# Kernel optimization log

Hardware: AMD Instinct MI355X
Metric: run time of the kernel (lower is better)

Reference implementation:

```python
import jax, jax.numpy as jnp
import numpy as np

EMB_DIM = 768
HEADS = 12
HEAD_DIM = EMB_DIM // HEADS  # 64


def setup_inputs() -> dict:
    key = jax.random.key(0)
    ks = jax.random.split(key, 9)
    s = 1.0 / np.sqrt(EMB_DIM)
    d = dict(
        x=jax.random.normal(ks[0], (2, 2048, EMB_DIM), dtype=jnp.float32),
        wq_w=jax.random.normal(ks[1], (EMB_DIM, EMB_DIM), dtype=jnp.float32) * s,
        wq_b=jax.random.normal(ks[2], (EMB_DIM,), dtype=jnp.float32) * 0.01,
        wk_w=jax.random.normal(ks[3], (EMB_DIM, EMB_DIM), dtype=jnp.float32) * s,
        wk_b=jax.random.normal(ks[4], (EMB_DIM,), dtype=jnp.float32) * 0.01,
        wv_w=jax.random.normal(ks[5], (EMB_DIM, EMB_DIM), dtype=jnp.float32) * s,
        wv_b=jax.random.normal(ks[6], (EMB_DIM,), dtype=jnp.float32) * 0.01,
        wo_w=jax.random.normal(ks[7], (EMB_DIM, EMB_DIM), dtype=jnp.float32) * s,
        wo_b=jax.random.normal(ks[8], (EMB_DIM,), dtype=jnp.float32) * 0.01,
    )
    return d


def reference(x, wq_w, wq_b, wk_w, wk_b, wv_w, wv_b, wo_w, wo_b):
    b, n, _ = x.shape
    # Linear projections (torch Linear: x @ W^T + b). q scaled by 1/8 == 1/sqrt(head_dim).
    q = (x @ wq_w.T + wq_b) / 8.0
    k = x @ wk_w.T + wk_b
    v = x @ wv_w.T + wv_b
    # [b, h, n, d]
    q = q.reshape(b, n, HEADS, HEAD_DIM).transpose(0, 2, 1, 3)
    k = k.reshape(b, n, HEADS, HEAD_DIM).transpose(0, 2, 1, 3)
    v = v.reshape(b, n, HEADS, HEAD_DIM).transpose(0, 2, 1, 3)
    # Full [b, h, n, n] score matrix with causal mask (strict upper triangle = -inf)
    scores = jnp.einsum('bhqd,bhkd->bhqk', q, k)
    causal = jnp.tril(jnp.ones((n, n), dtype=bool))  # True where allowed
    scores = jnp.where(causal[None, None], scores, -jnp.inf)
    attn = jax.nn.softmax(scores, axis=-1)
    out = jnp.einsum('bhqk,bhkd->bhqd', attn, v)
    out = out.transpose(0, 2, 1, 3).reshape(b, n, EMB_DIM)
    return out @ wo_w.T + wo_b
```

## Files before the change

### kernel.cpp

```cpp
#include <hip/hip_runtime.h>
#include <hip/hip_bf16.h>
#include <math.h>

#define EMB  768
#define NH   12
#define HD   64
#define SEQ  2048
#define BATCH 2
#define NTOK 4096

typedef __attribute__((ext_vector_type(8))) short short8;
typedef __attribute__((ext_vector_type(4))) float float4v;

static __device__ __forceinline__ short f2bf(float f) {
    __hip_bfloat16 h = __float2bfloat16(f);
    return *reinterpret_cast<short*>(&h);
}

static __device__ __forceinline__ void gll16(const void* g, void* l) {
    __builtin_amdgcn_global_load_lds(
        (const __attribute__((address_space(1))) void*)g,
        (__attribute__((address_space(3))) void*)l, 16, 0, 0);
}

__global__ __launch_bounds__(256) void cast_kernel(
    const float* __restrict__ x,  const float* __restrict__ wq,
    const float* __restrict__ wk, const float* __restrict__ wv,
    const float* __restrict__ wo,
    __hip_bfloat16* __restrict__ xb,  __hip_bfloat16* __restrict__ wqb,
    __hip_bfloat16* __restrict__ wkb, __hip_bfloat16* __restrict__ wvb,
    __hip_bfloat16* __restrict__ wob)
{
    const size_t S0 = (size_t)NTOK * EMB;
    const size_t S1 = (size_t)EMB * EMB;
    size_t i = ((size_t)blockIdx.x * 256 + threadIdx.x) * 8;
    const float* src; __hip_bfloat16* dst; size_t off;
    if      (i < S0)            { src = x;  dst = xb;  off = i; }
    else if (i < S0 + S1)       { src = wq; dst = wqb; off = i - S0; }
    else if (i < S0 + 2 * S1)   { src = wk; dst = wkb; off = i - S0 - S1; }
    else if (i < S0 + 3 * S1)   { src = wv; dst = wvb; off = i - S0 - 2 * S1; }
    else                        { src = wo; dst = wob; off = i - S0 - 3 * S1; }
    float4 f0 = *(const float4*)&src[off];
    float4 f1 = *(const float4*)&src[off + 4];
    short8 o;
    o[0] = f2bf(f0.x); o[1] = f2bf(f0.y); o[2] = f2bf(f0.z); o[3] = f2bf(f0.w);
    o[4] = f2bf(f1.x); o[5] = f2bf(f1.y); o[6] = f2bf(f1.z); o[7] = f2bf(f1.w);
    *(short8*)&dst[off] = o;
}

__global__ __launch_bounds__(256) void qkv_mfma_kernel(
    const __hip_bfloat16* __restrict__ xb,
    const __hip_bfloat16* __restrict__ wqb, const float* __restrict__ bq,
    const __hip_bfloat16* __restrict__ wkb, const float* __restrict__ bk,
    const __hip_bfloat16* __restrict__ wvb, const float* __restrict__ bv,
    __hip_bfloat16* __restrict__ q, __hip_bfloat16* __restrict__ k,
    __hip_bfloat16* __restrict__ vT)
{
    __shared__ __align__(16) short As[128 * 64];
    __shared__ __align__(16) short Bs[128 * 64];
    const int t = threadIdx.x;
    const int w = t >> 6, lane = t & 63;
    const int col = lane & 15, quad = lane >> 4;
    const int wm = w >> 1, wn = w & 1;
    const int m0 = blockIdx.y * 128;
    const int mat = blockIdx.x / 6;
    const int jj0 = (blockIdx.x % 6) * 128;
    const short* X = (const short*)xb;
    const short* W = (const short*)((mat == 0) ? wqb : (mat == 1) ? wkb : wvb);
    const float* bias = (mat == 0) ? bq : (mat == 1) ? bk : bv;

    float4v acc[4][4];
    #pragma unroll
    for (int mi = 0; mi < 4; ++mi)
        #pragma unroll
        for (int ni = 0; ni < 4; ++ni) acc[mi][ni] = (float4v){0.f, 0.f, 0.f, 0.f};

    for (int kb = 0; kb < EMB; kb += 64) {
        #pragma unroll
        for (int c = 0; c < 4; ++c) {
            int I = w * 256 + c * 64 + lane;
            int row = I >> 3;
            int c8 = (I & 7) ^ (row & 7);
            gll16(X + (size_t)(m0 + row) * EMB + kb + c8 * 8,
                  &As[(w * 256 + c * 64) * 8]);
            gll16(W + (size_t)(jj0 + row) * EMB + kb + c8 * 8,
                  &Bs[(w * 256 + c * 64) * 8]);
        }
        __syncthreads();
        #pragma unroll
        for (int ks = 0; ks < 2; ++ks) {
            short8 a[4], b[4];
            #pragma unroll
            for (int mi = 0; mi < 4; ++mi) {
                int row = wm * 64 + mi * 16 + col;
                a[mi] = *(short8*)&As[row * 64 + (((ks * 4 + quad) ^ (row & 7)) * 8)];
            }
            #pragma unroll
            for (int ni = 0; ni < 4; ++ni) {
                int row = wn * 64 + ni * 16 + col;
                b[ni] = *(short8*)&Bs[row * 64 + (((ks * 4 + quad) ^ (row & 7)) * 8)];
            }
            #pragma unroll
            for (int mi = 0; mi < 4; ++mi)
                #pragma unroll
                for (int ni = 0; ni < 4; ++ni)
                    acc[mi][ni] = __builtin_amdgcn_mfma_f32_16x16x32_bf16(
                        a[mi], b[ni], acc[mi][ni], 0, 0, 0);
        }
        __syncthreads();
    }
    const float scale = (mat == 0) ? 0.125f : 1.0f;
    __hip_bfloat16* dstqk = (mat == 0) ? q : k;
    #pragma unroll
    for (int mi = 0; mi < 4; ++mi) {
        #pragma unroll
        for (int ni = 0; ni < 4; ++ni) {
            int gj = jj0 + wn * 64 + ni * 16 + col;
            int h = gj >> 6, d = gj & 63;
            float bsv = bias[gj];
            #pragma unroll
            for (int r = 0; r < 4; ++r) {
                int gm = m0 + wm * 64 + mi * 16 + quad * 4 + r;
                int bi = gm >> 11, n = gm & (SEQ - 1);
                float val = (acc[mi][ni][r] + bsv) * scale;
                if (mat == 2)
                    vT[(((size_t)bi * NH + h) * HD + d) * SEQ + n] = __float2bfloat16(val);
                else
                    dstqk[(((size_t)bi * NH + h) * SEQ + n) * HD + d] = __float2bfloat16(val);
            }
        }
    }
}

__global__ __launch_bounds__(128) void attn_mfma_kernel(
    const __hip_bfloat16* __restrict__ qg, const __hip_bfloat16* __restrict__ kg,
    const __hip_bfloat16* __restrict__ vTg, __hip_bfloat16* __restrict__ ao)
{
    __shared__ __align__(16) short Ks[2][64 * 64];
    __shared__ __align__(16) short Vt[2][64 * 64];
    __shared__ __align__(16) short Ps[2][32][72];
    const int t = threadIdx.x;
    const int w = t >> 6, lane = t & 63;
    const int col = lane & 15, quad = lane >> 4;
    const int idx = blockIdx.x;
    const int qt = 31 - idx / 24;
    const int bh = idx % 24;
    const int q0 = qt * 64;
    const size_t base = (size_t)bh * SEQ * HD;
    const short* kp = (const short*)kg + base;
    const short* vp = (const short*)vTg + base;
    const short* qp = (const short*)qg + base;

    short8 qa[2][2];
    #pragma unroll
    for (int mi = 0; mi < 2; ++mi) {
        int qrow = q0 + w * 32 + mi * 16 + col;
        #pragma unroll
        for (int ks = 0; ks < 2; ++ks)
            qa[mi][ks] = *(const short8*)&qp[(size_t)qrow * HD + ks * 32 + quad * 8];
    }
    float4v accO[2][4];
    float lacc[2][4];
    #pragma unroll
    for (int mi = 0; mi < 2; ++mi) {
        #pragma unroll
        for (int di = 0; di < 4; ++di) accO[mi][di] = (float4v){0.f, 0.f, 0.f, 0.f};
        #pragma unroll
        for (int r = 0; r < 4; ++r) lacc[mi][r] = 0.f;
    }

    #pragma unroll
    for (int c = 0; c < 4; ++c) {
        int I = w * 256 + c * 64 + lane;
        int row = I >> 3;
        int c8 = (I & 7) ^ (row & 7);
        gll16(kp + (size_t)row * HD + c8 * 8, &Ks[0][(w * 256 + c * 64) * 8]);
        gll16(vp + (size_t)row * SEQ + c8 * 8, &Vt[0][(w * 256 + c * 64) * 8]);
    }

    for (int kt = 0; kt <= qt; ++kt) {
        const int cur = kt & 1;
        const int k0 = kt * 64;
        __syncthreads();
        if (kt < qt) {
            const int kn = k0 + 64;
            #pragma unroll
            for (int c = 0; c < 4; ++c) {
                int I = w * 256 + c * 64 + lane;
                int row = I >> 3;
                int c8 = (I & 7) ^ (row & 7);
                gll16(kp + (size_t)(kn + row) * HD + c8 * 8,
                      &Ks[cur ^ 1][(w * 256 + c * 64) * 8]);
                gll16(vp + (size_t)row * SEQ + kn + c8 * 8,
                      &Vt[cur ^ 1][(w * 256 + c * 64) * 8]);
            }
        }
        const short* Kc = &Ks[cur][0];
        const short* Vc = &Vt[cur][0];

        float4v s[2][4];
        #pragma unroll
        for (int mi = 0; mi < 2; ++mi)
            #pragma unroll
            for (int ni = 0; ni < 4; ++ni) s[mi][ni] = (float4v){0.f, 0.f, 0.f, 0.f};
        #pragma unroll
        for (int ks = 0; ks < 2; ++ks)
            #pragma unroll
            for (int ni = 0; ni < 4; ++ni) {
                int row = ni * 16 + col;
                short8 kf = *(short8*)&Kc[row * 64 + (((ks * 4 + quad) ^ (row & 7)) * 8)];
                #pragma unroll
                for (int mi = 0; mi < 2; ++mi)
                    s[mi][ni] = __builtin_amdgcn_mfma_f32_16x16x32_bf16(
                        qa[mi][ks], kf, s[mi][ni], 0, 0, 0);
            }

        if (kt == qt) {
            #pragma unroll
            for (int mi = 0; mi < 2; ++mi)
                #pragma unroll
                for (int ni = 0; ni < 4; ++ni) {
                    int gcol = k0 + ni * 16 + col;
                    #pragma unroll
                    for (int r = 0; r < 4; ++r) {
                        int grow = q0 + w * 32 + mi * 16 + quad * 4 + r;
                        s[mi][ni][r] = (gcol > grow) ? 0.f : __expf(s[mi][ni][r]);
                    }
                }
        } else {
            #pragma unroll
            for (int mi = 0; mi < 2; ++mi)
                #pragma unroll
                for (int ni = 0; ni < 4; ++ni)
                    #pragma unroll
                    for (int r = 0; r < 4; ++r)
                        s[mi][ni][r] = __expf(s[mi][ni][r]);
        }
        #pragma unroll
        for (int mi = 0; mi < 2; ++mi)
            #pragma unroll
            for (int r = 0; r < 4; ++r)
                lacc[mi][r] += (s[mi][0][r] + s[mi][1][r]) + (s[mi][2][r] + s[mi][3][r]);

        #pragma unroll
        for (int mi = 0; mi < 2; ++mi)
            #pragma unroll
            for (int ni = 0; ni < 4; ++ni)
                #pragma unroll
                for (int r = 0; r < 4; ++r)
                    Ps[w][mi * 16 + quad * 4 + r][ni * 16 + col] = f2bf(s[mi][ni][r]);
        short8 pa[2][2];
        #pragma unroll
        for (int mi = 0; mi < 2; ++mi)
            #pragma unroll
            for (int ks = 0; ks < 2; ++ks)
                pa[mi][ks] = *(short8*)&Ps[w][mi * 16 + col][ks * 32 + quad * 8];

        #pragma unroll
        for (int ks = 0; ks < 2; ++ks)
            #pragma unroll
            for (int di = 0; di < 4; ++di) {
                int row = di * 16 + col;
                short8 vf = *(short8*)&Vc[row * 64 + (((ks * 4 + quad) ^ (row & 7)) * 8)];
                #pragma unroll
                for (int mi = 0; mi < 2; ++mi)
                    accO[mi][di] = __builtin_amdgcn_mfma_f32_16x16x32_bf16(
                        pa[mi][ks], vf, accO[mi][di], 0, 0, 0);
            }
    }

    #pragma unroll
    for (int msk = 1; msk < 16; msk <<= 1)
        #pragma unroll
        for (int mi = 0; mi < 2; ++mi)
            #pragma unroll
            for (int r = 0; r < 4; ++r)
                lacc[mi][r] += __shfl_xor(lacc[mi][r], msk);
    const int bi = bh / NH, h = bh % NH;
    #pragma unroll
    for (int mi = 0; mi < 2; ++mi)
        #pragma unroll
        for (int r = 0; r < 4; ++r) {
            float inv = 1.0f / lacc[mi][r];
            int n = q0 + w * 32 + mi * 16 + quad * 4 + r;
            #pragma unroll
            for (int di = 0; di < 4; ++di)
                ao[((size_t)bi * SEQ + n) * EMB + h * HD + di * 16 + col] =
                    __float2bfloat16(accO[mi][di][r] * inv);
        }
}

__global__ __launch_bounds__(256) void out_proj_mfma_kernel(
    const __hip_bfloat16* __restrict__ a, const __hip_bfloat16* __restrict__ wob,
    const float* __restrict__ bias, float* __restrict__ out)
{
    __shared__ __align__(16) short As[64 * 64];
    __shared__ __align__(16) short Bs[128 * 64];
    const int t = threadIdx.x;
    const int w = t >> 6, lane = t & 63;
    const int col = lane & 15, quad = lane >> 4;
    const int m0 = blockIdx.y * 64;
    const int n0 = blockIdx.x * 128;
    const short* A = (const short*)a;
    const short* W = (const short*)wob;

    float4v acc[4][2];
    #pragma unroll
    for (int mi = 0; mi < 4; ++mi)
        #pragma unroll
        for (int ni = 0; ni < 2; ++ni) acc[mi][ni] = (float4v){0.f, 0.f, 0.f, 0.f};

    for (int kb = 0; kb < EMB; kb += 64) {
        #pragma unroll
        for (int c = 0; c < 2; ++c) {
            int I = w * 128 + c * 64 + lane;
            int row = I >> 3;
            int c8 = (I & 7) ^ (row & 7);
            gll16(A + (size_t)(m0 + row) * EMB + kb + c8 * 8,
                  &As[(w * 128 + c * 64) * 8]);
        }
        #pragma unroll
        for (int c = 0; c < 4; ++c) {
            int I = w * 256 + c * 64 + lane;
            int row = I >> 3;
            int c8 = (I & 7) ^ (row & 7);
            gll16(W + (size_t)(n0 + row) * EMB + kb + c8 * 8,
                  &Bs[(w * 256 + c * 64) * 8]);
        }
        __syncthreads();
        #pragma unroll
        for (int ks = 0; ks < 2; ++ks) {
            short8 av[4], bv[2];
            #pragma unroll
            for (int mi = 0; mi < 4; ++mi) {
                int row = mi * 16 + col;
                av[mi] = *(short8*)&As[row * 64 + (((ks * 4 + quad) ^ (row & 7)) * 8)];
            }
            #pragma unroll
            for (int ni = 0; ni < 2; ++ni) {
                int row = w * 32 + ni * 16 + col;
                bv[ni] = *(short8*)&Bs[row * 64 + (((ks * 4 + quad) ^ (row & 7)) * 8)];
            }
            #pragma unroll
            for (int mi = 0; mi < 4; ++mi)
                #pragma unroll
                for (int ni = 0; ni < 2; ++ni)
                    acc[mi][ni] = __builtin_amdgcn_mfma_f32_16x16x32_bf16(
                        av[mi], bv[ni], acc[mi][ni], 0, 0, 0);
        }
        __syncthreads();
    }
    #pragma unroll
    for (int mi = 0; mi < 4; ++mi)
        #pragma unroll
        for (int ni = 0; ni < 2; ++ni) {
            int gj = n0 + w * 32 + ni * 16 + col;
            float bsv = bias[gj];
            #pragma unroll
            for (int r = 0; r < 4; ++r) {
                int gm = m0 + mi * 16 + quad * 4 + r;
                out[(size_t)gm * EMB + gj] = acc[mi][ni][r] + bsv;
            }
        }
}

extern "C" void kernel_launch(void* const* d_in, const int* in_sizes, int n_in,
                              void* d_out, int out_size, void* d_ws, size_t ws_size,
                              hipStream_t stream) {
    const float* x  = (const float*)d_in[0];
    const float* wq = (const float*)d_in[1];
    const float* bq = (const float*)d_in[2];
    const float* wk = (const float*)d_in[3];
    const float* bk = (const float*)d_in[4];
    const float* wv = (const float*)d_in[5];
    const float* bv = (const float*)d_in[6];
    const float* wo = (const float*)d_in[7];
    const float* bo = (const float*)d_in[8];
    float* out = (float*)d_out;

    const size_t TOK = (size_t)NTOK * EMB;
    const size_t WSZ = (size_t)EMB * EMB;
    __hip_bfloat16* xb  = (__hip_bfloat16*)d_ws;
    __hip_bfloat16* wqb = xb  + TOK;
    __hip_bfloat16* wkb = wqb + WSZ;
    __hip_bfloat16* wvb = wkb + WSZ;
    __hip_bfloat16* wob = wvb + WSZ;
    __hip_bfloat16* qb  = wob + WSZ;
    __hip_bfloat16* kb  = qb  + TOK;
    __hip_bfloat16* vTb = kb  + TOK;
    __hip_bfloat16* aob = vTb + TOK;

    cast_kernel<<<2688, 256, 0, stream>>>(x, wq, wk, wv, wo, xb, wqb, wkb, wvb, wob);
    qkv_mfma_kernel<<<dim3(18, 32), 256, 0, stream>>>(xb, wqb, bq, wkb, bk, wvb, bv,
                                                      qb, kb, vTb);
    attn_mfma_kernel<<<768, 128, 0, stream>>>(qb, kb, vTb, aob);
    out_proj_mfma_kernel<<<dim3(6, 64), 256, 0, stream>>>(aob, wob, bo, out);
}
```

Baseline: 186.2 us.

## Split long causal query tiles across two KV halves and stage V-transpose stores

Query tiles 16-31 now have their KV range split into two halves handled by separate blocks, capping per-block work at 16 KV tiles. The partial unnormalized outputs and row sums go to fp32 scratch, and a new combine kernel merges and normalizes them. This is meant to fix the load imbalance of the causal workload. Separately, the V projection epilogue transposes through LDS so the vT stores become coalesced 16-byte writes instead of scattered 2-byte ones. The cost is extra fp32 scratch traffic, one more kernel launch, and scratch buffers that reuse workspace regions.

```diff
diff --git a/kernel.cpp b/kernel.cpp
--- a/kernel.cpp
+++ b/kernel.cpp
@@ -56,8 +56,9 @@
     __hip_bfloat16* __restrict__ q, __hip_bfloat16* __restrict__ k,
     __hip_bfloat16* __restrict__ vT)
 {
-    __shared__ __align__(16) short As[128 * 64];
-    __shared__ __align__(16) short Bs[128 * 64];
+    __shared__ __align__(16) short SM[16384];
+    short* As = SM;
+    short* Bs = SM + 8192;
     const int t = threadIdx.x;
     const int w = t >> 6, lane = t & 63;
     const int col = lane & 15, quad = lane >> 4;
@@ -109,32 +110,59 @@
         }
         __syncthreads();
     }
-    const float scale = (mat == 0) ? 0.125f : 1.0f;
-    __hip_bfloat16* dstqk = (mat == 0) ? q : k;
-    #pragma unroll
-    for (int mi = 0; mi < 4; ++mi) {
-        #pragma unroll
-        for (int ni = 0; ni < 4; ++ni) {
-            int gj = jj0 + wn * 64 + ni * 16 + col;
-            int h = gj >> 6, d = gj & 63;
-            float bsv = bias[gj];
-            #pragma unroll
-            for (int r = 0; r < 4; ++r) {
-                int gm = m0 + wm * 64 + mi * 16 + quad * 4 + r;
-                int bi = gm >> 11, n = gm & (SEQ - 1);
-                float val = (acc[mi][ni][r] + bsv) * scale;
-                if (mat == 2)
-                    vT[(((size_t)bi * NH + h) * HD + d) * SEQ + n] = __float2bfloat16(val);
-                else
-                    dstqk[(((size_t)bi * NH + h) * SEQ + n) * HD + d] = __float2bfloat16(val);
-            }
+    const int bi = m0 >> 11, n0g = m0 & (SEQ - 1);
+    if (mat != 2) {
+        const float scale = (mat == 0) ? 0.125f : 1.0f;
+        __hip_bfloat16* dstqk = (mat == 0) ? q : k;
+        #pragma unroll
+        for (int mi = 0; mi < 4; ++mi) {
+            #pragma unroll
+            for (int ni = 0; ni < 4; ++ni) {
+                int gj = jj0 + wn * 64 + ni * 16 + col;
+                int h = gj >> 6, d = gj & 63;
+                float bsv = bias[gj];
+                #pragma unroll
+                for (int r = 0; r < 4; ++r) {
+                    int gm = m0 + wm * 64 + mi * 16 + quad * 4 + r;
+                    int bb = gm >> 11, n = gm & (SEQ - 1);
+                    dstqk[(((size_t)bb * NH + h) * SEQ + n) * HD + d] =
+                        __float2bfloat16((acc[mi][ni][r] + bsv) * scale);
+                }
+            }
+        }
+    } else {
+        #pragma unroll
+        for (int mi = 0; mi < 4; ++mi)
+            #pragma unroll
+            for (int ni = 0; ni < 4; ++ni) {
+                int d_l = wn * 64 + ni * 16 + col;
+                float bsv = bias[jj0 + d_l];
+                #pragma unroll
+                for (int r = 0; r < 4; ++r) {
+                    int n_l = wm * 64 + mi * 16 + quad * 4 + r;
+                    SM[(d_l << 7) + ((((n_l >> 3) ^ col) << 3) | (n_l & 7))] =
+                        f2bf(acc[mi][ni][r] + bsv);
+                }
+            }
+        __syncthreads();
+        #pragma unroll
+        for (int it = 0; it < 8; ++it) {
+            int I = it * 256 + t;
+            int d_l = I >> 4, c8 = I & 15;
+            short8 val = *(short8*)&SM[(d_l << 7) + (c8 << 3)];
+            int n_l = (c8 ^ (d_l & 15)) << 3;
+            int gj = jj0 + d_l;
+            int h = gj >> 6, dd = gj & 63;
+            *(short8*)&vT[(((size_t)bi * NH + h) * HD + dd) * SEQ + n0g + n_l] = val;
         }
     }
 }
 
 __global__ __launch_bounds__(128) void attn_mfma_kernel(
     const __hip_bfloat16* __restrict__ qg, const __hip_bfloat16* __restrict__ kg,
-    const __hip_bfloat16* __restrict__ vTg, __hip_bfloat16* __restrict__ ao)
+    const __hip_bfloat16* __restrict__ vTg, __hip_bfloat16* __restrict__ ao,
+    float* __restrict__ Os0, float* __restrict__ Os1,
+    float* __restrict__ l0, float* __restrict__ l1)
 {
     __shared__ __align__(16) short Ks[2][64 * 64];
     __shared__ __align__(16) short Vt[2][64 * 64];
@@ -142,9 +170,20 @@
     const int t = threadIdx.x;
     const int w = t >> 6, lane = t & 63;
     const int col = lane & 15, quad = lane >> 4;
-    const int idx = blockIdx.x;
-    const int qt = 31 - idx / 24;
-    const int bh = idx % 24;
+    const int id = blockIdx.x;
+    const int bh = id % 24;
+    const int x = id / 24;
+    int qt, c;
+    if (x < 16) { qt = 16 + x; c = 0; }
+    else {
+        int i = x - 16, j = i >> 1;
+        if ((i & 1) == 0) { qt = 31 - j; c = 1; }
+        else              { qt = 15 - j; c = 0; }
+    }
+    const int kt0 = c * 16;
+    const int ktend = (kt0 + 16 < qt + 1) ? kt0 + 16 : qt + 1;
+    const int niter = ktend - kt0;
+    const bool single = (qt <= 15);
     const int q0 = qt * 64;
     const size_t base = (size_t)bh * SEQ * HD;
     const short* kp = (const short*)kg + base;
@@ -169,30 +208,34 @@
         for (int r = 0; r < 4; ++r) lacc[mi][r] = 0.f;
     }
 
-    #pragma unroll
-    for (int c = 0; c < 4; ++c) {
-        int I = w * 256 + c * 64 + lane;
-        int row = I >> 3;
-        int c8 = (I & 7) ^ (row & 7);
-        gll16(kp + (size_t)row * HD + c8 * 8, &Ks[0][(w * 256 + c * 64) * 8]);
-        gll16(vp + (size_t)row * SEQ + c8 * 8, &Vt[0][(w * 256 + c * 64) * 8]);
-    }
-
-    for (int kt = 0; kt <= qt; ++kt) {
-        const int cur = kt & 1;
+    {
+        const int k0 = kt0 * 64;
+        #pragma unroll
+        for (int cc = 0; cc < 4; ++cc) {
+            int I = w * 256 + cc * 64 + lane;
+            int row = I >> 3;
+            int c8 = (I & 7) ^ (row & 7);
+            gll16(kp + (size_t)(k0 + row) * HD + c8 * 8, &Ks[0][(w * 256 + cc * 64) * 8]);
+            gll16(vp + (size_t)row * SEQ + k0 + c8 * 8, &Vt[0][(w * 256 + cc * 64) * 8]);
+        }
+    }
+
+    for (int lk = 0; lk < niter; ++lk) {
+        const int kt = kt0 + lk;
+        const int cur = lk & 1;
         const int k0 = kt * 64;
         __syncthreads();
-        if (kt < qt) {
+        if (lk + 1 < niter) {
             const int kn = k0 + 64;
             #pragma unroll
-            for (int c = 0; c < 4; ++c) {
-                int I = w * 256 + c * 64 + lane;
+            for (int cc = 0; cc < 4; ++cc) {
+                int I = w * 256 + cc * 64 + lane;
                 int row = I >> 3;
                 int c8 = (I & 7) ^ (row & 7);
                 gll16(kp + (size_t)(kn + row) * HD + c8 * 8,
-                      &Ks[cur ^ 1][(w * 256 + c * 64) * 8]);
+                      &Ks[cur ^ 1][(w * 256 + cc * 64) * 8]);
                 gll16(vp + (size_t)row * SEQ + kn + c8 * 8,
-                      &Vt[cur ^ 1][(w * 256 + c * 64) * 8]);
+                      &Vt[cur ^ 1][(w * 256 + cc * 64) * 8]);
             }
         }
         const short* Kc = &Ks[cur][0];
@@ -276,18 +319,60 @@
             #pragma unroll
             for (int r = 0; r < 4; ++r)
                 lacc[mi][r] += __shfl_xor(lacc[mi][r], msk);
+
     const int bi = bh / NH, h = bh % NH;
-    #pragma unroll
-    for (int mi = 0; mi < 2; ++mi)
-        #pragma unroll
-        for (int r = 0; r < 4; ++r) {
-            float inv = 1.0f / lacc[mi][r];
-            int n = q0 + w * 32 + mi * 16 + quad * 4 + r;
-            #pragma unroll
-            for (int di = 0; di < 4; ++di)
-                ao[((size_t)bi * SEQ + n) * EMB + h * HD + di * 16 + col] =
-                    __float2bfloat16(accO[mi][di][r] * inv);
-        }
+    if (single) {
+        #pragma unroll
+        for (int mi = 0; mi < 2; ++mi)
+            #pragma unroll
+            for (int r = 0; r < 4; ++r) {
+                float inv = 1.0f / lacc[mi][r];
+                int n = q0 + w * 32 + mi * 16 + quad * 4 + r;
+                #pragma unroll
+                for (int di = 0; di < 4; ++di)
+                    ao[((size_t)bi * SEQ + n) * EMB + h * HD + di * 16 + col] =
+                        __float2bfloat16(accO[mi][di][r] * inv);
+            }
+    } else {
+        float* Os = c ? Os1 : Os0;
+        float* ls = c ? l1 : l0;
+        #pragma unroll
+        for (int mi = 0; mi < 2; ++mi)
+            #pragma unroll
+            for (int r = 0; r < 4; ++r) {
+                int n = q0 + w * 32 + mi * 16 + quad * 4 + r;
+                int nn = n - 1024;
+                size_t rowb = ((size_t)bi * 1024 + nn) * EMB + h * HD;
+                #pragma unroll
+                for (int di = 0; di < 4; ++di)
+                    Os[rowb + di * 16 + col] = accO[mi][di][r];
+                if (col == 0)
+                    ls[((size_t)bi * 1024 + nn) * NH + h] = lacc[mi][r];
+            }
+    }
+}
+
+__global__ __launch_bounds__(256) void combine_kernel(
+    const float* __restrict__ Os0, const float* __restrict__ Os1,
+    const float* __restrict__ l0, const float* __restrict__ l1,
+    __hip_bfloat16* __restrict__ ao)
+{
+    size_t e8 = ((size_t)blockIdx.x * 256 + threadIdx.x) * 8;
+    int u = e8 / EMB;
+    int within = e8 % EMB;
+    int h = within >> 6;
+    int bi = u >> 10, nn = u & 1023;
+    float inv = 1.0f / (l0[(size_t)u * NH + h] + l1[(size_t)u * NH + h]);
+    float4 a0 = *(const float4*)&Os0[e8];
+    float4 a1 = *(const float4*)&Os0[e8 + 4];
+    float4 b0 = *(const float4*)&Os1[e8];
+    float4 b1 = *(const float4*)&Os1[e8 + 4];
+    short8 o;
+    o[0] = f2bf((a0.x + b0.x) * inv); o[1] = f2bf((a0.y + b0.y) * inv);
+    o[2] = f2bf((a0.z + b0.z) * inv); o[3] = f2bf((a0.w + b0.w) * inv);
+    o[4] = f2bf((a1.x + b1.x) * inv); o[5] = f2bf((a1.y + b1.y) * inv);
+    o[6] = f2bf((a1.z + b1.z) * inv); o[7] = f2bf((a1.w + b1.w) * inv);
+    *(short8*)&ao[((size_t)bi * SEQ + 1024 + nn) * EMB + within] = o;
 }
 
 __global__ __launch_bounds__(256) void out_proj_mfma_kernel(
@@ -389,10 +474,15 @@
     __hip_bfloat16* kb  = qb  + TOK;
     __hip_bfloat16* vTb = kb  + TOK;
     __hip_bfloat16* aob = vTb + TOK;
+    float* Os0 = (float*)d_ws;
+    float* Os1 = (float*)(aob + TOK);
+    float* l0  = Os1 + (size_t)2 * 1024 * EMB;
+    float* l1  = l0  + (size_t)2 * 1024 * NH;
 
     cast_kernel<<<2688, 256, 0, stream>>>(x, wq, wk, wv, wo, xb, wqb, wkb, wvb, wob);
     qkv_mfma_kernel<<<dim3(18, 32), 256, 0, stream>>>(xb, wqb, bq, wkb, bk, wvb, bv,
                                                       qb, kb, vTb);
-    attn_mfma_kernel<<<768, 128, 0, stream>>>(qb, kb, vTb, aob);
+    attn_mfma_kernel<<<1152, 128, 0, stream>>>(qb, kb, vTb, aob, Os0, Os1, l0, l1);
+    combine_kernel<<<768, 256, 0, stream>>>(Os0, Os1, l0, l1, aob);
     out_proj_mfma_kernel<<<dim3(6, 64), 256, 0, stream>>>(aob, wob, bo, out);
 }
```

After: 172.0 us. -7.7%, faster.
